# Kernel tuning notes

Hardware: AMD Instinct MI355X
Metric: run time of the kernel (lower is better)

## Reference

```python
import jax, jax.numpy as jnp
import numpy as np

B, S, D_IN, D_OUT, H = 2, 2048, 1024, 1024, 16
HD = D_OUT // H  # 64


def setup_inputs() -> dict:
    key = jax.random.key(0)
    ks = jax.random.split(key, 6)
    s = 0.02
    return {
        "x": jax.random.normal(ks[0], (B, S, D_IN), dtype=jnp.float32),
        "W_q": jax.random.normal(ks[1], (D_IN, D_OUT), dtype=jnp.float32) * s,
        "W_k": jax.random.normal(ks[2], (D_IN, D_OUT), dtype=jnp.float32) * s,
        "W_v": jax.random.normal(ks[3], (D_IN, D_OUT), dtype=jnp.float32) * s,
        "W_o": jax.random.normal(ks[4], (D_OUT, D_OUT), dtype=jnp.float32) * s,
        "b_o": jax.random.normal(ks[5], (D_OUT,), dtype=jnp.float32) * s,
    }


def reference(x, W_q, W_k, W_v, W_o, b_o):
    b, n, _ = x.shape
    # project and split heads: [b, h, n, hd]
    q = (x @ W_q).reshape(b, n, H, HD).transpose(0, 2, 1, 3)
    k = (x @ W_k).reshape(b, n, H, HD).transpose(0, 2, 1, 3)
    v = (x @ W_v).reshape(b, n, H, HD).transpose(0, 2, 1, 3)
    scores = jnp.einsum("bhqd,bhkd->bhqk", q, k) / jnp.sqrt(jnp.float32(HD))
    causal = jnp.tril(jnp.ones((n, n), dtype=bool))
    scores = jnp.where(causal, scores, -jnp.inf)
    attn = jax.nn.softmax(scores, axis=-1)  # dropout p=0.0 -> identity
    ctx = jnp.einsum("bhqk,bhkd->bhqd", attn, v)
    ctx = ctx.transpose(0, 2, 1, 3).reshape(b, n, D_OUT)
    return ctx @ W_o + b_o
```

## Files before the change

### kernel.cpp

```cpp
#include <hip/hip_runtime.h>

#define B_    2
#define S_    2048
#define DIN   1024
#define DOUT  1024
#define H_    16
#define HD_   64
#define M_    (B_ * S_)

typedef __bf16 bf16x8 __attribute__((ext_vector_type(8)));
typedef float  f32x4  __attribute__((ext_vector_type(4)));

__device__ __forceinline__ f32x4 MFMA(bf16x8 a, bf16x8 b, f32x4 c) {
    return __builtin_amdgcn_mfma_f32_16x16x32_bf16(a, b, c, 0, 0, 0);
}

__device__ __forceinline__ unsigned short f2b(float f) {
    union { float f; unsigned int u; } v; v.f = f;
    unsigned int u = v.u;
    return (unsigned short)((u + 0x7fffu + ((u >> 16) & 1u)) >> 16);
}

__device__ __forceinline__ unsigned pack2(float a, float b) {
    union { __bf16 h[2]; unsigned u; } cv;
    cv.h[0] = (__bf16)a; cv.h[1] = (__bf16)b;
    return cv.u;
}

#define GLDS(gp, lp) __builtin_amdgcn_global_load_lds( \
    (const __attribute__((address_space(1))) void*)(gp), \
    (__attribute__((address_space(3))) void*)(lp), 16, 0, 0)

#define QSCALE 0.1803368801111204f

__global__ __launch_bounds__(256) void k_cvt_all(const float* __restrict__ x,
                                                 const float* __restrict__ Wq,
                                                 const float* __restrict__ Wk,
                                                 const float* __restrict__ Wv,
                                                 const float* __restrict__ Wo,
                                                 unsigned short* __restrict__ xb,
                                                 unsigned short* __restrict__ WqkvT,
                                                 unsigned short* __restrict__ WoT) {
    __shared__ float tile[32][33];
    int bid = blockIdx.x;
    if (bid < 4096) {
        int i = (bid * 256 + threadIdx.x) * 4;
        float4 v = *reinterpret_cast<const float4*>(x + i);
        ushort4 o;
        o.x = f2b(v.x); o.y = f2b(v.y); o.z = f2b(v.z); o.w = f2b(v.w);
        *reinterpret_cast<ushort4*>(xb + i) = o;
        return;
    }
    int wb = bid - 4096;
    int w = wb >> 10;
    int t = wb & 1023;
    const float* src = (w == 0) ? Wq : (w == 1) ? Wk : (w == 2) ? Wv : Wo;
    unsigned short* dst = (w < 3) ? WqkvT + (size_t)w * 1024 * DIN : WoT;
    int n0 = (t & 31) * 32, k0 = (t >> 5) * 32;
    int tx = threadIdx.x & 31, ty = threadIdx.x >> 5;
    for (int i = 0; i < 4; i++)
        tile[ty + i * 8][tx] = src[(size_t)(k0 + ty + i * 8) * DOUT + n0 + tx];
    __syncthreads();
    for (int i = 0; i < 4; i++)
        dst[(size_t)(n0 + ty + i * 8) * DIN + k0 + tx] = f2b(tile[tx][ty + i * 8]);
}

__global__ __launch_bounds__(256) void k_trV(const unsigned short* __restrict__ V,
                                             unsigned short* __restrict__ Vt) {
    __shared__ unsigned short tile[64][72];
    int st = blockIdx.x, bh = blockIdx.y;
    int b = bh >> 4, h = bh & 15;
    int t = threadIdx.x;
    int r = t >> 2, c = (t & 3) << 4;
    const unsigned short* src = V + (size_t)(b * S_ + st * 64 + r) * DOUT + h * HD_ + c;
    *reinterpret_cast<int4*>(&tile[r][c])     = *reinterpret_cast<const int4*>(src);
    *reinterpret_cast<int4*>(&tile[r][c + 8]) = *reinterpret_cast<const int4*>(src + 8);
    __syncthreads();
    unsigned short o[16];
    for (int j = 0; j < 16; j++) o[j] = tile[c + j][r];
    unsigned short* dst = Vt + (size_t)(bh * 64 + r) * S_ + st * 64 + c;
    *reinterpret_cast<int4*>(dst)     = *reinterpret_cast<int4*>(&o[0]);
    *reinterpret_cast<int4*>(dst + 8) = *reinterpret_cast<int4*>(&o[8]);
}

template <int OUT_MODE>
__global__ __launch_bounds__(256) void k_gemm(const unsigned short* __restrict__ A,
                                              const unsigned short* __restrict__ Bt,
                                              unsigned short* __restrict__ Cq,
                                              unsigned short* __restrict__ Ck,
                                              unsigned short* __restrict__ Cv,
                                              float* __restrict__ Cf,
                                              const float* __restrict__ bias,
                                              int M, int N, int K, int nbx) {
    __shared__ __align__(16) unsigned short As[128 * 64];
    __shared__ __align__(16) unsigned short Bs[128 * 64];

    int nwg = gridDim.x;
    int chunkw = nwg >> 3;
    int bid = blockIdx.x;
    int nid = (bid & 7) * chunkw + (bid >> 3);
    int by = nid / nbx, bx = nid - by * nbx;
    int m0 = by * 128, n0 = bx * 128;

    int tid = threadIdx.x;
    int wid = tid >> 6, lane = tid & 63;
    int wm = wid >> 1, wn = wid & 1;
    int lr = lane & 15, lg = lane >> 4;

    f32x4 acc[4][4] = {};

    int srow = lane >> 3;
    int scol = ((lane & 7) ^ srow) * 8;
    int rsw  = lr & 7;

    for (int k0 = 0; k0 < K; k0 += 64) {
#pragma unroll
        for (int c = 0; c < 4; c++) {
            int chunk = wid * 4 + c;
            int row = chunk * 8 + srow;
            GLDS(A  + (size_t)(m0 + row) * K + k0 + scol, (char*)As + chunk * 1024);
            GLDS(Bt + (size_t)(n0 + row) * K + k0 + scol, (char*)Bs + chunk * 1024);
        }
        __syncthreads();

#pragma unroll
        for (int kk = 0; kk < 2; kk++) {
            bf16x8 af[4], bf[4];
#pragma unroll
            for (int mi = 0; mi < 4; mi++)
                af[mi] = *reinterpret_cast<const bf16x8*>(
                    &As[(wm * 64 + mi * 16 + lr) * 64 + (((kk * 4 + lg) ^ rsw) * 8)]);
#pragma unroll
            for (int ni = 0; ni < 4; ni++)
                bf[ni] = *reinterpret_cast<const bf16x8*>(
                    &Bs[(wn * 64 + ni * 16 + lr) * 64 + (((kk * 4 + lg) ^ rsw) * 8)]);
#pragma unroll
            for (int mi = 0; mi < 4; mi++)
#pragma unroll
                for (int ni = 0; ni < 4; ni++)
                    acc[mi][ni] = MFMA(af[mi], bf[ni], acc[mi][ni]);
        }
        __syncthreads();
    }

    for (int mi = 0; mi < 4; mi++)
        for (int ni = 0; ni < 4; ni++)
            for (int i = 0; i < 4; i++) {
                int row = m0 + wm * 64 + mi * 16 + lg * 4 + i;
                int col = n0 + wn * 64 + ni * 16 + lr;
                float v = acc[mi][ni][i];
                if (OUT_MODE == 2) {
                    Cf[(size_t)row * N + col] = v + bias[col];
                } else {
                    if (col < 1024)       Cq[(size_t)row * 1024 + col] = f2b(v * QSCALE);
                    else if (col < 2048)  Ck[(size_t)row * 1024 + (col - 1024)] = f2b(v);
                    else                  Cv[(size_t)row * 1024 + (col - 2048)] = f2b(v);
                }
            }
}

__global__ __launch_bounds__(512, 4) void k_attn(const unsigned short* __restrict__ Q,
                                                 const unsigned short* __restrict__ Kg,
                                                 const unsigned short* __restrict__ Vt,
                                                 unsigned short* __restrict__ ctx) {
    int p = blockIdx.x;
    int bh = blockIdx.y;
    int b = bh >> 4, h = bh & 15;
    int tid = threadIdx.x, wid = tid >> 6, lane = tid & 63;
    int lr = lane & 15, lg = lane >> 4;
    int qtB = 31 - p;
    int qt = (wid < 4) ? qtB : p;
    int q0 = qt * 64 + (wid & 3) * 16;

    __shared__ __align__(16) unsigned short Ks[2][64 * 64];
    __shared__ __align__(16) unsigned short Vs[2][64 * 64];
    __shared__ __align__(16) unsigned p_lds32[8][16 * 32];
    unsigned* pl32 = p_lds32[wid];

    const unsigned short* Qp = Q  + (size_t)b * S_ * DOUT + (size_t)h * HD_;
    const unsigned short* Kp = Kg + (size_t)b * S_ * DOUT + (size_t)h * HD_;
    const unsigned short* Vp = Vt + (size_t)(b * H_ + h) * HD_ * S_;

    bf16x8 qf0 = *reinterpret_cast<const bf16x8*>(&Qp[(size_t)(q0 + lr) * DOUT + lg * 8]);
    bf16x8 qf1 = *reinterpret_cast<const bf16x8*>(&Qp[(size_t)(q0 + lr) * DOUT + 32 + lg * 8]);
    asm volatile("" : "+v"(qf0), "+v"(qf1));

    int srow = lane >> 3;
    int scol = ((lane & 7) ^ srow) * 8;

#define STAGE_KV(buf, t)                                                           \
    {                                                                              \
        int kv0_ = (t) * 64;                                                       \
        int krow = wid * 8 + srow;                                                 \
        GLDS(Kp + (size_t)(kv0_ + krow) * DOUT + scol,                             \
             (char*)&Ks[buf][0] + wid * 1024);                                     \
        GLDS(Vp + (size_t)krow * S_ + kv0_ + scol,                                 \
             (char*)&Vs[buf][0] + wid * 1024);                                     \
    }

    STAGE_KV(0, 0)

    f32x4 o[4] = {};
    float l = 0.f;

    int ntile = qtB + 1;
    int rxor = (lr & 7) << 4;
    int qg = q0 + lr;

    for (int t = 0; t < ntile; t++) {
        int cur = t & 1;
        if (t + 1 < ntile) {
            STAGE_KV(cur ^ 1, t + 1)
            asm volatile("s_waitcnt vmcnt(2)" ::: "memory");
        } else {
            asm volatile("s_waitcnt vmcnt(0)" ::: "memory");
        }
        __builtin_amdgcn_s_barrier();

        if (t <= qt) {
            const unsigned short* Kt = Ks[cur];
            const unsigned short* Vl = Vs[cur];
            int kv0 = t * 64;

            f32x4 s[4] = {};
            __builtin_amdgcn_s_setprio(1);
#pragma unroll
            for (int nf = 0; nf < 4; nf++)
#pragma unroll
                for (int kk = 0; kk < 2; kk++) {
                    bf16x8 kf = *reinterpret_cast<const bf16x8*>(
                        &Kt[(nf * 16 + lr) * 64 + (((kk * 64 + lg * 16) ^ rxor) >> 1)]);
                    s[nf] = MFMA(kf, kk ? qf1 : qf0, s[nf]);
                }
            __builtin_amdgcn_s_setprio(0);

            if (t == qt) {
#pragma unroll
                for (int nf = 0; nf < 4; nf++)
#pragma unroll
                    for (int i = 0; i < 4; i++)
                        if (kv0 + nf * 16 + lg * 4 + i > qg) s[nf][i] = -2000.0f;
            }

            f32x4 acc = {};
#pragma unroll
            for (int nf = 0; nf < 4; nf++) {
                f32x4 pv;
#pragma unroll
                for (int i = 0; i < 4; i++) pv[i] = exp2f(s[nf][i]);
                acc += pv;
                unsigned w0 = pack2(pv[0], pv[1]);
                unsigned w1 = pack2(pv[2], pv[3]);
                int unit = (nf * 2 + (lg >> 1)) ^ (lr & 7);
                uint2 wd; wd.x = w0; wd.y = w1;
                *reinterpret_cast<uint2*>(&pl32[lr * 32 + unit * 4 + (lg & 1) * 2]) = wd;
            }
            l += (acc[0] + acc[1]) + (acc[2] + acc[3]);

            bf16x8 pf[2];
#pragma unroll
            for (int kvb = 0; kvb < 2; kvb++)
                pf[kvb] = *reinterpret_cast<const bf16x8*>(
                    &pl32[lr * 32 + (((kvb * 4 + lg) ^ (lr & 7)) * 4)]);

            __builtin_amdgcn_s_setprio(1);
#pragma unroll
            for (int nd = 0; nd < 4; nd++)
#pragma unroll
                for (int kk = 0; kk < 2; kk++) {
                    bf16x8 vf = *reinterpret_cast<const bf16x8*>(
                        &Vl[(nd * 16 + lr) * 64 + (((kk * 64 + lg * 16) ^ rxor) >> 1)]);
                    o[nd] = MFMA(pf[kk], vf, o[nd]);
                }
            __builtin_amdgcn_s_setprio(0);
        }

        __builtin_amdgcn_s_barrier();
    }

    l += __shfl_xor(l, 16, 64);
    l += __shfl_xor(l, 32, 64);

#pragma unroll
    for (int i = 0; i < 4; i++) {
        float li = __shfl(l, lg * 4 + i, 16);
        float r = __builtin_amdgcn_rcpf(li);
#pragma unroll
        for (int nd = 0; nd < 4; nd++)
            ((__bf16*)ctx)[((size_t)b * S_ + q0 + lg * 4 + i) * DOUT + h * HD_ + nd * 16 + lr] =
                (__bf16)(o[nd][i] * r);
    }
#undef STAGE_KV
}

extern "C" void kernel_launch(void* const* d_in, const int* in_sizes, int n_in,
                              void* d_out, int out_size, void* d_ws, size_t ws_size,
                              hipStream_t stream) {
    const float* x  = (const float*)d_in[0];
    const float* Wq = (const float*)d_in[1];
    const float* Wk = (const float*)d_in[2];
    const float* Wv = (const float*)d_in[3];
    const float* Wo = (const float*)d_in[4];
    const float* bo = (const float*)d_in[5];
    float* out = (float*)d_out;
    char* ws = (char*)d_ws;
    const size_t MB = 1u << 20;

    unsigned short* xb    = (unsigned short*)(ws);
    unsigned short* Vtb   = (unsigned short*)(ws);
    unsigned short* WqkvT = (unsigned short*)(ws + 8 * MB);
    unsigned short* WoT   = (unsigned short*)(ws + 14 * MB);
    unsigned short* Qb    = (unsigned short*)(ws + 16 * MB);
    unsigned short* Kb    = (unsigned short*)(ws + 24 * MB);
    unsigned short* Vb    = (unsigned short*)(ws + 32 * MB);
    unsigned short* ctx   = Vb;

    (void)in_sizes; (void)n_in; (void)out_size; (void)ws_size;

    k_cvt_all<<<8192, 256, 0, stream>>>(x, Wq, Wk, Wv, Wo, xb, WqkvT, WoT);

    k_gemm<0><<<768, 256, 0, stream>>>(xb, WqkvT, Qb, Kb, Vb, nullptr, nullptr,
                                       M_, 3072, DIN, 24);

    dim3 gt(S_ / 64, B_ * H_);
    k_trV<<<gt, 256, 0, stream>>>(Vb, Vtb);

    dim3 ga(16, B_ * H_);
    k_attn<<<ga, 512, 0, stream>>>(Qb, Kb, Vtb, ctx);

    k_gemm<2><<<256, 256, 0, stream>>>(ctx, WoT, nullptr, nullptr, nullptr,
                                       out, bo, M_, DOUT, DOUT, 8);
}
```

Before: 120.8 us.

## Deepen attention KV prefetch, widen convert tiles, shrink output GEMM M-tile

Attention now uses a 4-slot KV ring buffer with two tiles prefetched ahead and drops the per-iteration barrier, aiming to hide more load latency. The convert kernel moves to 64x64 transpose tiles with vectorized loads and stores and handles four x chunks per block, so it launches fewer blocks. The output projection GEMM is templated on BM and uses 64-row tiles, doubling its grid to 512 blocks for better CU occupancy. Removing the barrier is only safe if the ring depth keeps a slot from being overwritten while another wave still reads it. The larger LDS footprint in attention may also lower occupancy.

```diff
diff --git a/kernel.cpp b/kernel.cpp
--- a/kernel.cpp
+++ b/kernel.cpp
@@ -41,28 +41,44 @@
                                                  unsigned short* __restrict__ xb,
                                                  unsigned short* __restrict__ WqkvT,
                                                  unsigned short* __restrict__ WoT) {
-    __shared__ float tile[32][33];
+    __shared__ __align__(16) float tile[64][68];
     int bid = blockIdx.x;
-    if (bid < 4096) {
-        int i = (bid * 256 + threadIdx.x) * 4;
-        float4 v = *reinterpret_cast<const float4*>(x + i);
-        ushort4 o;
-        o.x = f2b(v.x); o.y = f2b(v.y); o.z = f2b(v.z); o.w = f2b(v.w);
-        *reinterpret_cast<ushort4*>(xb + i) = o;
+    int tid = threadIdx.x;
+    if (bid < 1024) {
+#pragma unroll
+        for (int j = 0; j < 4; j++) {
+            int i = bid * 4096 + j * 1024 + tid * 4;
+            float4 v = *reinterpret_cast<const float4*>(x + i);
+            ushort4 o;
+            o.x = f2b(v.x); o.y = f2b(v.y); o.z = f2b(v.z); o.w = f2b(v.w);
+            *reinterpret_cast<ushort4*>(xb + i) = o;
+        }
         return;
     }
-    int wb = bid - 4096;
-    int w = wb >> 10;
-    int t = wb & 1023;
+    int wb = bid - 1024;
+    int w = wb >> 8;
+    int t = wb & 255;
     const float* src = (w == 0) ? Wq : (w == 1) ? Wk : (w == 2) ? Wv : Wo;
     unsigned short* dst = (w < 3) ? WqkvT + (size_t)w * 1024 * DIN : WoT;
-    int n0 = (t & 31) * 32, k0 = (t >> 5) * 32;
-    int tx = threadIdx.x & 31, ty = threadIdx.x >> 5;
-    for (int i = 0; i < 4; i++)
-        tile[ty + i * 8][tx] = src[(size_t)(k0 + ty + i * 8) * DOUT + n0 + tx];
+    int k0 = (t >> 4) * 64, n0 = (t & 15) * 64;
+#pragma unroll
+    for (int j = 0; j < 4; j++) {
+        int idx = j * 256 + tid;
+        int r = idx >> 4, c4 = (idx & 15) * 4;
+        *reinterpret_cast<float4*>(&tile[r][c4]) =
+            *reinterpret_cast<const float4*>(&src[(size_t)(k0 + r) * DOUT + n0 + c4]);
+    }
     __syncthreads();
-    for (int i = 0; i < 4; i++)
-        dst[(size_t)(n0 + ty + i * 8) * DIN + k0 + tx] = f2b(tile[tx][ty + i * 8]);
+#pragma unroll
+    for (int j = 0; j < 2; j++) {
+        int idx = j * 256 + tid;
+        int n = idx >> 3, gk = (idx & 7) * 8;
+        unsigned short o[8];
+#pragma unroll
+        for (int u = 0; u < 8; u++) o[u] = f2b(tile[gk + u][n]);
+        *reinterpret_cast<int4*>(&dst[(size_t)(n0 + n) * DIN + k0 + gk]) =
+            *reinterpret_cast<int4*>(o);
+    }
 }
 
 __global__ __launch_bounds__(256) void k_trV(const unsigned short* __restrict__ V,
@@ -83,7 +99,7 @@
     *reinterpret_cast<int4*>(dst + 8) = *reinterpret_cast<int4*>(&o[8]);
 }
 
-template <int OUT_MODE>
+template <int OUT_MODE, int BM>
 __global__ __launch_bounds__(256) void k_gemm(const unsigned short* __restrict__ A,
                                               const unsigned short* __restrict__ Bt,
                                               unsigned short* __restrict__ Cq,
@@ -92,7 +108,8 @@
                                               float* __restrict__ Cf,
                                               const float* __restrict__ bias,
                                               int M, int N, int K, int nbx) {
-    __shared__ __align__(16) unsigned short As[128 * 64];
+    constexpr int MI = BM / 32;
+    __shared__ __align__(16) unsigned short As[BM * 64];
     __shared__ __align__(16) unsigned short Bs[128 * 64];
 
     int nwg = gridDim.x;
@@ -100,14 +117,14 @@
     int bid = blockIdx.x;
     int nid = (bid & 7) * chunkw + (bid >> 3);
     int by = nid / nbx, bx = nid - by * nbx;
-    int m0 = by * 128, n0 = bx * 128;
+    int m0 = by * BM, n0 = bx * 128;
 
     int tid = threadIdx.x;
     int wid = tid >> 6, lane = tid & 63;
     int wm = wid >> 1, wn = wid & 1;
     int lr = lane & 15, lg = lane >> 4;
 
-    f32x4 acc[4][4] = {};
+    f32x4 acc[MI][4] = {};
 
     int srow = lane >> 3;
     int scol = ((lane & 7) ^ srow) * 8;
@@ -115,27 +132,32 @@
 
     for (int k0 = 0; k0 < K; k0 += 64) {
 #pragma unroll
+        for (int c = 0; c < MI; c++) {
+            int chunk = wid * MI + c;
+            int row = chunk * 8 + srow;
+            GLDS(A + (size_t)(m0 + row) * K + k0 + scol, (char*)As + chunk * 1024);
+        }
+#pragma unroll
         for (int c = 0; c < 4; c++) {
             int chunk = wid * 4 + c;
             int row = chunk * 8 + srow;
-            GLDS(A  + (size_t)(m0 + row) * K + k0 + scol, (char*)As + chunk * 1024);
             GLDS(Bt + (size_t)(n0 + row) * K + k0 + scol, (char*)Bs + chunk * 1024);
         }
         __syncthreads();
 
 #pragma unroll
         for (int kk = 0; kk < 2; kk++) {
-            bf16x8 af[4], bf[4];
-#pragma unroll
-            for (int mi = 0; mi < 4; mi++)
+            bf16x8 af[MI], bf[4];
+#pragma unroll
+            for (int mi = 0; mi < MI; mi++)
                 af[mi] = *reinterpret_cast<const bf16x8*>(
-                    &As[(wm * 64 + mi * 16 + lr) * 64 + (((kk * 4 + lg) ^ rsw) * 8)]);
+                    &As[(wm * (BM / 2) + mi * 16 + lr) * 64 + (((kk * 4 + lg) ^ rsw) * 8)]);
 #pragma unroll
             for (int ni = 0; ni < 4; ni++)
                 bf[ni] = *reinterpret_cast<const bf16x8*>(
                     &Bs[(wn * 64 + ni * 16 + lr) * 64 + (((kk * 4 + lg) ^ rsw) * 8)]);
 #pragma unroll
-            for (int mi = 0; mi < 4; mi++)
+            for (int mi = 0; mi < MI; mi++)
 #pragma unroll
                 for (int ni = 0; ni < 4; ni++)
                     acc[mi][ni] = MFMA(af[mi], bf[ni], acc[mi][ni]);
@@ -143,10 +165,10 @@
         __syncthreads();
     }
 
-    for (int mi = 0; mi < 4; mi++)
+    for (int mi = 0; mi < MI; mi++)
         for (int ni = 0; ni < 4; ni++)
             for (int i = 0; i < 4; i++) {
-                int row = m0 + wm * 64 + mi * 16 + lg * 4 + i;
+                int row = m0 + wm * (BM / 2) + mi * 16 + lg * 4 + i;
                 int col = n0 + wn * 64 + ni * 16 + lr;
                 float v = acc[mi][ni][i];
                 if (OUT_MODE == 2) {
@@ -172,8 +194,8 @@
     int qt = (wid < 4) ? qtB : p;
     int q0 = qt * 64 + (wid & 3) * 16;
 
-    __shared__ __align__(16) unsigned short Ks[2][64 * 64];
-    __shared__ __align__(16) unsigned short Vs[2][64 * 64];
+    __shared__ __align__(16) unsigned short Ks[4][64 * 64];
+    __shared__ __align__(16) unsigned short Vs[4][64 * 64];
     __shared__ __align__(16) unsigned p_lds32[8][16 * 32];
     unsigned* pl32 = p_lds32[wid];
 
@@ -198,19 +220,22 @@
              (char*)&Vs[buf][0] + wid * 1024);                                     \
     }
 
+    int ntile = qtB + 1;
     STAGE_KV(0, 0)
+    STAGE_KV(1, 1)
 
     f32x4 o[4] = {};
     float l = 0.f;
-
-    int ntile = qtB + 1;
     int rxor = (lr & 7) << 4;
     int qg = q0 + lr;
 
+    int cur = 0;
     for (int t = 0; t < ntile; t++) {
-        int cur = t & 1;
-        if (t + 1 < ntile) {
-            STAGE_KV(cur ^ 1, t + 1)
+        int ahead = ntile - 1 - t;
+        if (ahead >= 2) {
+            STAGE_KV((cur + 2) & 3, t + 2)
+            asm volatile("s_waitcnt vmcnt(4)" ::: "memory");
+        } else if (ahead == 1) {
             asm volatile("s_waitcnt vmcnt(2)" ::: "memory");
         } else {
             asm volatile("s_waitcnt vmcnt(0)" ::: "memory");
@@ -249,10 +274,8 @@
 #pragma unroll
                 for (int i = 0; i < 4; i++) pv[i] = exp2f(s[nf][i]);
                 acc += pv;
-                unsigned w0 = pack2(pv[0], pv[1]);
-                unsigned w1 = pack2(pv[2], pv[3]);
                 int unit = (nf * 2 + (lg >> 1)) ^ (lr & 7);
-                uint2 wd; wd.x = w0; wd.y = w1;
+                uint2 wd; wd.x = pack2(pv[0], pv[1]); wd.y = pack2(pv[2], pv[3]);
                 *reinterpret_cast<uint2*>(&pl32[lr * 32 + unit * 4 + (lg & 1) * 2]) = wd;
             }
             l += (acc[0] + acc[1]) + (acc[2] + acc[3]);
@@ -275,7 +298,7 @@
             __builtin_amdgcn_s_setprio(0);
         }
 
-        __builtin_amdgcn_s_barrier();
+        cur = (cur + 1) & 3;
     }
 
     l += __shfl_xor(l, 16, 64);
@@ -317,10 +340,10 @@
 
     (void)in_sizes; (void)n_in; (void)out_size; (void)ws_size;
 
-    k_cvt_all<<<8192, 256, 0, stream>>>(x, Wq, Wk, Wv, Wo, xb, WqkvT, WoT);
-
-    k_gemm<0><<<768, 256, 0, stream>>>(xb, WqkvT, Qb, Kb, Vb, nullptr, nullptr,
-                                       M_, 3072, DIN, 24);
+    k_cvt_all<<<2048, 256, 0, stream>>>(x, Wq, Wk, Wv, Wo, xb, WqkvT, WoT);
+
+    k_gemm<0, 128><<<768, 256, 0, stream>>>(xb, WqkvT, Qb, Kb, Vb, nullptr, nullptr,
+                                            M_, 3072, DIN, 24);
 
     dim3 gt(S_ / 64, B_ * H_);
     k_trV<<<gt, 256, 0, stream>>>(Vb, Vtb);
@@ -328,6 +351,6 @@
     dim3 ga(16, B_ * H_);
     k_attn<<<ga, 512, 0, stream>>>(Qb, Kb, Vtb, ctx);
 
-    k_gemm<2><<<256, 256, 0, stream>>>(ctx, WoT, nullptr, nullptr, nullptr,
-                                       out, bo, M_, DOUT, DOUT, 8);
-}
+    k_gemm<2, 64><<<512, 256, 0, stream>>>(ctx, WoT, nullptr, nullptr, nullptr,
+                                           out, bo, M_, DOUT, DOUT, 8);
+}
```

New measurement: 113.6 us. 6.0% less time.
